# Kernel optimization log

Hardware: AMD Instinct MI355X
Metric: run time of the kernel (lower is better)

Reference implementation:

```python
import jax, jax.numpy as jnp
import numpy as np

INPUTDIM = 256
OUTDIM = 256
GRIDSIZE = 300
SCALE_BASE = 1.0
SCALE_FOURIER = 1.0
BATCH = 2048


def setup_inputs() -> dict:
    key = jax.random.key(0)
    k_x, k_bw, k_fc = jax.random.split(key, 3)
    x = jax.random.normal(k_x, (BATCH, INPUTDIM), dtype=jnp.float32)
    # HeUniform for base_weight: limit = sqrt(6 / fan_in)
    limit = np.sqrt(6.0 / INPUTDIM)
    base_weight = jax.random.uniform(
        k_bw, (INPUTDIM, OUTDIM), dtype=jnp.float32, minval=-limit, maxval=limit)
    stddev = 1.0 / (np.sqrt(INPUTDIM) * np.sqrt(GRIDSIZE))
    fouriercoeffs = (jax.random.normal(k_fc, (2, OUTDIM, INPUTDIM, GRIDSIZE), dtype=jnp.float32)
                     * jnp.float32(stddev))
    return {"x": x, "base_weight": base_weight, "fouriercoeffs": fouriercoeffs}


def reference(x, base_weight, fouriercoeffs):
    # Base path: silu(x @ W)
    base_output = jax.nn.silu(x @ base_weight)  # [B, J]
    # Fourier feature expansion: k = 1..gridsize
    k = jnp.arange(1, GRIDSIZE + 1, dtype=x.dtype)  # [K]
    theta = x[:, :, None] * k[None, None, :]        # [B, I, K]
    c = jnp.cos(theta)
    s = jnp.sin(theta)
    # einsum 'dbik,djik->bj' split into cos and sin parts
    fourier_output = (jnp.einsum('bik,jik->bj', c, fouriercoeffs[0])
                      + jnp.einsum('bik,jik->bj', s, fouriercoeffs[1]))
    return SCALE_BASE * base_output + SCALE_FOURIER * fourier_output
```

## Files before the change

### kernel.cpp

```cpp
#include <hip/hip_runtime.h>
#include <hip/hip_bf16.h>
#include <cstdint>

#define BATCH   2048
#define INDIM   256
#define OUTDIM  256
#define KGRID   300
#define NCHUNK  10

typedef __attribute__((ext_vector_type(4))) float f32x4;
typedef __attribute__((ext_vector_type(8))) short bf16x8;

__device__ __forceinline__ uint32_t pack_bf16x2(float lo, float hi) {
    union { __hip_bfloat162 h; uint32_t u; } cv;
    cv.h = __float22bfloat162_rn(make_float2(lo, hi));
    return cv.u;
}

__device__ __forceinline__ void load_lds16(const void* g, void* l) {
    __builtin_amdgcn_global_load_lds(
        (const __attribute__((address_space(1))) void*)g,
        (__attribute__((address_space(3))) void*)l, 16, 0, 0);
}

#define PACKED_U4 ((size_t)INDIM * NCHUNK * OUTDIM * 8)
#define PACKED_BYTES (PACKED_U4 * 16)

__global__ __launch_bounds__(256) void pack_kernel(
    const float* __restrict__ fc, uint4* __restrict__ pk)
{
    size_t tidg = (size_t)blockIdx.x * 256 + threadIdx.x;
    int sub = tidg & 7;
    int j   = (tidg >> 3) & 255;
    int ich = (int)(tidg >> 11);
    int ch  = ich % NCHUNK;
    int i   = ich / NCHUNK;
    int kb  = ch * 32 + (sub ^ (j & 7)) * 4;
    if (kb > KGRID - 4) kb = KGRID - 4;
    const float* pc = fc + ((size_t)j * INDIM + i) * KGRID + kb;
    const float* ps = pc + (size_t)OUTDIM * INDIM * KGRID;
    float4 vc = *reinterpret_cast<const float4*>(pc);
    float4 vs = *reinterpret_cast<const float4*>(ps);
    uint4 wv;
    wv.x = pack_bf16x2(vc.x, vs.x);
    wv.y = pack_bf16x2(vc.y, vs.y);
    wv.z = pack_bf16x2(vc.z, vs.z);
    wv.w = pack_bf16x2(vc.w, vs.w);
    pk[tidg] = wv;
}

__global__ __launch_bounds__(256, 2) void fourier_dma_kernel(
    const float* __restrict__ x, const uint4* __restrict__ pk,
    float* __restrict__ part)
{
    __shared__ uint4 Abuf[2][128][8];
    __shared__ uint4 Bbuf[2][128][8];

    const int tid = threadIdx.x;
    const int flat = blockIdx.x + (blockIdx.y << 3) + (blockIdx.z << 4);
    const int L  = (flat & 7) * 64 + (flat >> 3);
    const int b0 = (L & 7) * 256;
    const int j0 = ((L >> 3) & 1) * 128;
    const int z  = L >> 4;
    const int i0 = z * 8;

    const int lane = tid & 63, wave = tid >> 6;
    const int wm = wave >> 1, wn = wave & 1;
    const int lrow = lane & 15, lgrp = lane >> 4;
    const int grow = tid >> 1,  gh = tid & 1;
    const int q4 = wave * 4;

    f32x4 acc[2][4][4] = {};
    float thc[2], thn[2], c1[2], s1[2], t2[2];

    thn[0] = x[(size_t)(b0 + grow) * INDIM + i0];
    thn[1] = x[(size_t)(b0 + 128 + grow) * INDIM + i0];

    {
        const uint4* src = pk + ((size_t)(i0 * NCHUNK) * 256 + j0) * 8;
        #pragma unroll
        for (int q = 0; q < 4; ++q)
            load_lds16(src + (q4 + q) * 64 + lane,
                       (char*)&Bbuf[0][0][0] + (q4 + q) * 1024);
    }

    int il = 0, ch = 0;
    #pragma unroll 1
    for (int t = 0; t < 8 * NCHUNK; ++t) {
        if (ch == 0) {
            thc[0] = thn[0]; thc[1] = thn[1];
            #pragma unroll
            for (int m = 0; m < 2; ++m) {
                __sincosf(thc[m], &s1[m], &c1[m]);
                t2[m] = 2.f * c1[m];
            }
            int iln = (il + 1 < 8) ? il + 1 : il;
            thn[0] = x[(size_t)(b0 + grow) * INDIM + i0 + iln];
            thn[1] = x[(size_t)(b0 + 128 + grow) * INDIM + i0 + iln];
        }
        {
            int il2 = il, ch2 = ch + 1;
            if (ch2 == NCHUNK) { ch2 = 0; il2 = (il + 1 < 8) ? il + 1 : il; }
            const uint4* src =
                pk + ((size_t)((i0 + il2) * NCHUNK + ch2) * 256 + j0) * 8;
            char* dst = (char*)&Bbuf[(t + 1) & 1][0][0];
            #pragma unroll
            for (int q = 0; q < 4; ++q)
                load_lds16(src + (q4 + q) * 64 + lane, dst + (q4 + q) * 1024);
        }
        #pragma unroll
        for (int m = 0; m < 2; ++m) {
            const int k0 = ch * 32 + gh * 16;
            float ck, sk;
            __sincosf(thc[m] * (float)(k0 + 1), &sk, &ck);
            float cp = __builtin_fmaf(ck, c1[m],  sk * s1[m]);
            float sp = __builtin_fmaf(sk, c1[m], -ck * s1[m]);
            const int swz = grow & 7;
            #pragma unroll
            for (int c = 0; c < 4; ++c) {
                uint32_t uu[4];
                #pragma unroll
                for (int qq = 0; qq < 4; ++qq) {
                    uu[qq] = pack_bf16x2(ck, sk);
                    float cn = __builtin_fmaf(t2[m], ck, -cp);
                    float sn = __builtin_fmaf(t2[m], sk, -sp);
                    cp = ck; sp = sk; ck = cn; sk = sn;
                }
                if (ch == NCHUNK - 1) {
                    #pragma unroll
                    for (int qq = 0; qq < 4; ++qq)
                        if (k0 + c * 4 + qq >= KGRID) uu[qq] = 0u;
                }
                Abuf[m][grow][(gh * 4 + c) ^ swz] =
                    make_uint4(uu[0], uu[1], uu[2], uu[3]);
            }
        }
        __syncthreads();
        __builtin_amdgcn_s_setprio(1);
        #pragma unroll
        for (int s = 0; s < 2; ++s) {
            bf16x8 bfr[4];
            #pragma unroll
            for (int nf = 0; nf < 4; ++nf) {
                const int jl = wn * 64 + nf * 16 + lrow;
                uint4 tv = Bbuf[t & 1][jl][(s * 4 + lgrp) ^ (jl & 7)];
                bfr[nf] = *reinterpret_cast<bf16x8*>(&tv);
            }
            #pragma unroll
            for (int m = 0; m < 2; ++m) {
                #pragma unroll
                for (int mf = 0; mf < 4; ++mf) {
                    const int rowA = wm * 64 + mf * 16 + lrow;
                    uint4 tv = Abuf[m][rowA][(s * 4 + lgrp) ^ (rowA & 7)];
                    bf16x8 af = *reinterpret_cast<bf16x8*>(&tv);
                    #pragma unroll
                    for (int nf = 0; nf < 4; ++nf)
                        acc[m][mf][nf] = __builtin_amdgcn_mfma_f32_16x16x32_bf16(
                            af, bfr[nf], acc[m][mf][nf], 0, 0, 0);
                }
            }
        }
        __builtin_amdgcn_s_setprio(0);
        __syncthreads();
        if (++ch == NCHUNK) { ch = 0; ++il; }
    }

    float* pws = part + (size_t)z * BATCH * OUTDIM;
    #pragma unroll
    for (int m = 0; m < 2; ++m)
        #pragma unroll
        for (int mf = 0; mf < 4; ++mf)
            #pragma unroll
            for (int nf = 0; nf < 4; ++nf)
                #pragma unroll
                for (int r = 0; r < 4; ++r) {
                    int b = b0 + m * 128 + wm * 64 + mf * 16 + lgrp * 4 + r;
                    int j = j0 + wn * 64 + nf * 16 + lrow;
                    pws[(size_t)b * OUTDIM + j] = acc[m][mf][nf][r];
                }
}

__global__ __launch_bounds__(256, 2) void fourier_kernel_fb(
    const float* __restrict__ x, const float* __restrict__ fc,
    float* __restrict__ ws, int ips)
{
    __shared__ uint4 Abuf[2][128][8];
    __shared__ uint4 Bbuf[128][8];

    const int tid  = threadIdx.x;
    const int b0   = blockIdx.x * 256;
    const int j0   = blockIdx.y * 128;
    const int i0   = blockIdx.z * ips;

    const int lane = tid & 63, wave = tid >> 6;
    const int wm   = wave >> 1, wn = wave & 1;
    const int lrow = lane & 15, lgrp = lane >> 4;
    const int grow = tid >> 1,  gh = tid & 1;

    f32x4 acc[2][4][4] = {};

    #pragma unroll 1
    for (int il = 0; il < ips; ++il) {
        const int i = i0 + il;
        float th[2], c1[2], s1[2], t2[2];
        th[0] = x[(size_t)(b0 + grow)       * INDIM + i];
        th[1] = x[(size_t)(b0 + 128 + grow) * INDIM + i];
        #pragma unroll
        for (int m = 0; m < 2; ++m) {
            __sincosf(th[m], &s1[m], &c1[m]);
            t2[m] = 2.f * c1[m];
        }
        #pragma unroll 1
        for (int ch = 0; ch < NCHUNK; ++ch) {
            #pragma unroll
            for (int r = 0; r < 4; ++r) {
                int flat = r * 256 + tid;
                int jl = flat >> 3, sub = flat & 7;
                int kb = ch * 32 + sub * 4;
                if (kb > KGRID - 4) kb = KGRID - 4;
                const float* pc = fc + ((size_t)(j0 + jl) * INDIM + i) * KGRID + kb;
                const float* ps = pc + (size_t)OUTDIM * INDIM * KGRID;
                float4 vc = *reinterpret_cast<const float4*>(pc);
                float4 vs = *reinterpret_cast<const float4*>(ps);
                uint4 wv;
                wv.x = pack_bf16x2(vc.x, vs.x);
                wv.y = pack_bf16x2(vc.y, vs.y);
                wv.z = pack_bf16x2(vc.z, vs.z);
                wv.w = pack_bf16x2(vc.w, vs.w);
                Bbuf[jl][sub ^ (jl & 7)] = wv;
            }
            #pragma unroll
            for (int m = 0; m < 2; ++m) {
                const int k0 = ch * 32 + gh * 16;
                float ck, sk;
                __sincosf(th[m] * (float)(k0 + 1), &sk, &ck);
                float cp = __builtin_fmaf(ck, c1[m],  sk * s1[m]);
                float sp = __builtin_fmaf(sk, c1[m], -ck * s1[m]);
                const int swz = grow & 7;
                #pragma unroll
                for (int c = 0; c < 4; ++c) {
                    uint32_t uu[4];
                    #pragma unroll
                    for (int qq = 0; qq < 4; ++qq) {
                        const int kidx = k0 + c * 4 + qq;
                        float cc = (kidx < KGRID) ? ck : 0.f;
                        float ss = (kidx < KGRID) ? sk : 0.f;
                        uu[qq] = pack_bf16x2(cc, ss);
                        float cn = __builtin_fmaf(t2[m], ck, -cp);
                        float sn = __builtin_fmaf(t2[m], sk, -sp);
                        cp = ck; sp = sk; ck = cn; sk = sn;
                    }
                    Abuf[m][grow][(gh * 4 + c) ^ swz] =
                        make_uint4(uu[0], uu[1], uu[2], uu[3]);
                }
            }
            __syncthreads();
            #pragma unroll
            for (int s = 0; s < 2; ++s) {
                bf16x8 bfr[4];
                #pragma unroll
                for (int nf = 0; nf < 4; ++nf) {
                    const int jl = wn * 64 + nf * 16 + lrow;
                    uint4 tv = Bbuf[jl][(s * 4 + lgrp) ^ (jl & 7)];
                    bfr[nf] = *reinterpret_cast<bf16x8*>(&tv);
                }
                #pragma unroll
                for (int m = 0; m < 2; ++m) {
                    #pragma unroll
                    for (int mf = 0; mf < 4; ++mf) {
                        const int rowA = wm * 64 + mf * 16 + lrow;
                        uint4 tv = Abuf[m][rowA][(s * 4 + lgrp) ^ (rowA & 7)];
                        bf16x8 af = *reinterpret_cast<bf16x8*>(&tv);
                        #pragma unroll
                        for (int nf = 0; nf < 4; ++nf)
                            acc[m][mf][nf] = __builtin_amdgcn_mfma_f32_16x16x32_bf16(
                                af, bfr[nf], acc[m][mf][nf], 0, 0, 0);
                    }
                }
            }
            __syncthreads();
        }
    }

    float* pws = ws + (size_t)blockIdx.z * BATCH * OUTDIM;
    #pragma unroll
    for (int m = 0; m < 2; ++m)
        #pragma unroll
        for (int mf = 0; mf < 4; ++mf)
            #pragma unroll
            for (int nf = 0; nf < 4; ++nf)
                #pragma unroll
                for (int r = 0; r < 4; ++r) {
                    int b = b0 + m * 128 + wm * 64 + mf * 16 + lgrp * 4 + r;
                    int j = j0 + wn * 64 + nf * 16 + lrow;
                    pws[(size_t)b * OUTDIM + j] = acc[m][mf][nf][r];
                }
}

__global__ __launch_bounds__(256) void combine_kernel(
    const float* __restrict__ x, const float* __restrict__ w,
    const float* __restrict__ part, float* __restrict__ out, int nsplit)
{
    __shared__ float Xs[64][16];
    __shared__ float Wt[16][68];

    const int tid = threadIdx.x;
    const int b0 = blockIdx.x * 64;
    const int j0 = blockIdx.y * 64;
    const int tx = tid & 15, ty = tid >> 4;

    float acc[4][4] = {};

    for (int kb = 0; kb < INDIM; kb += 16) {
        {
            int m = tid >> 2, kq = (tid & 3) * 4;
            float4 v = *reinterpret_cast<const float4*>(
                &x[(size_t)(b0 + m) * INDIM + kb + kq]);
            Xs[m][kq+0] = v.x; Xs[m][kq+1] = v.y; Xs[m][kq+2] = v.z; Xs[m][kq+3] = v.w;
        }
        {
            int kr = tid >> 4, jc = (tid & 15) * 4;
            float4 v = *reinterpret_cast<const float4*>(
                &w[(size_t)(kb + kr) * OUTDIM + j0 + jc]);
            Wt[kr][jc+0] = v.x; Wt[kr][jc+1] = v.y; Wt[kr][jc+2] = v.z; Wt[kr][jc+3] = v.w;
        }
        __syncthreads();
        #pragma unroll
        for (int kk = 0; kk < 16; ++kk) {
            float a[4], b[4];
            #pragma unroll
            for (int q = 0; q < 4; ++q) { a[q] = Xs[ty*4+q][kk]; b[q] = Wt[kk][tx*4+q]; }
            #pragma unroll
            for (int q = 0; q < 4; ++q)
                #pragma unroll
                for (int p = 0; p < 4; ++p)
                    acc[q][p] = __builtin_fmaf(a[q], b[p], acc[q][p]);
        }
        __syncthreads();
    }

    float psum[4][4] = {};
    for (int s = 0; s < nsplit; ++s) {
        const float* base = part + (size_t)s * BATCH * OUTDIM;
        #pragma unroll
        for (int q = 0; q < 4; ++q) {
            float4 pv = *reinterpret_cast<const float4*>(
                &base[(size_t)(b0 + ty*4 + q) * OUTDIM + j0 + tx*4]);
            psum[q][0] += pv.x; psum[q][1] += pv.y;
            psum[q][2] += pv.z; psum[q][3] += pv.w;
        }
    }

    #pragma unroll
    for (int q = 0; q < 4; ++q)
        #pragma unroll
        for (int p = 0; p < 4; ++p) {
            float v = acc[q][p];
            float sv = v / (1.f + __expf(-v));
            out[(size_t)(b0 + ty*4 + q) * OUTDIM + (j0 + tx*4 + p)] =
                sv + psum[q][p];
        }
}

extern "C" void kernel_launch(void* const* d_in, const int* in_sizes, int n_in,
                              void* d_out, int out_size, void* d_ws, size_t ws_size,
                              hipStream_t stream) {
    const float* x  = (const float*)d_in[0];
    const float* bw = (const float*)d_in[1];
    const float* fc = (const float*)d_in[2];
    float* out = (float*)d_out;

    const size_t per = (size_t)BATCH * OUTDIM * sizeof(float);

    if (ws_size >= PACKED_BYTES + 32 * per) {
        uint4* pk   = (uint4*)d_ws;
        float* part = (float*)((char*)d_ws + PACKED_BYTES);
        pack_kernel<<<(int)(PACKED_U4 / 256), 256, 0, stream>>>(fc, pk);
        fourier_dma_kernel<<<dim3(8, 2, 32), 256, 0, stream>>>(x, pk, part);
        combine_kernel<<<dim3(BATCH / 64, OUTDIM / 64), 256, 0, stream>>>(
            x, bw, part, out, 32);
    } else {
        float* part = (float*)d_ws;
        int S = 32;
        while (S > 1 && (size_t)S * per > ws_size) S >>= 1;
        const int ips = INDIM / S;
        fourier_kernel_fb<<<dim3(BATCH / 256, OUTDIM / 128, S), 256, 0, stream>>>(
            x, fc, part, ips);
        combine_kernel<<<dim3(BATCH / 64, OUTDIM / 64), 256, 0, stream>>>(
            x, bw, part, out, S);
    }
}
```

Before: 244.5 us.

## Retile Fourier GEMM to 128 batch rows by full 256 outputs, pack FMA recurrence

Changes the block tile from 256 batch rows by 128 outputs to 128 batch rows by all 256 outputs. Each block now generates cos/sin features for only 128 rows, so the transcendental and recurrence work is no longer repeated across two output-column blocks. The cost is twice the B-operand traffic per block, now streamed for all 256 columns into a larger double-buffered LDS. It also advances the Chebyshev recurrence for cos and sin together with one packed v_pk_fma_f32 per step.

```diff
diff --git a/kernel.cpp b/kernel.cpp
--- a/kernel.cpp
+++ b/kernel.cpp
@@ -9,12 +9,20 @@
 #define NCHUNK  10
 
 typedef __attribute__((ext_vector_type(4))) float f32x4;
+typedef __attribute__((ext_vector_type(2))) float f32x2;
 typedef __attribute__((ext_vector_type(8))) short bf16x8;
 
 __device__ __forceinline__ uint32_t pack_bf16x2(float lo, float hi) {
     union { __hip_bfloat162 h; uint32_t u; } cv;
     cv.h = __float22bfloat162_rn(make_float2(lo, hi));
     return cv.u;
+}
+
+__device__ __forceinline__ f32x2 pk_fma_sub(f32x2 a, f32x2 b, f32x2 c) {
+    f32x2 d;
+    asm("v_pk_fma_f32 %0, %1, %2, %3 neg_lo:[0,0,1] neg_hi:[0,0,1]"
+        : "=v"(d) : "v"(a), "v"(b), "v"(c));
+    return d;
 }
 
 __device__ __forceinline__ void load_lds16(const void* g, void* l) {
@@ -53,14 +61,13 @@
     const float* __restrict__ x, const uint4* __restrict__ pk,
     float* __restrict__ part)
 {
-    __shared__ uint4 Abuf[2][128][8];
-    __shared__ uint4 Bbuf[2][128][8];
+    __shared__ uint4 Abuf[128][8];
+    __shared__ uint4 Bbuf[2][256][8];
 
     const int tid = threadIdx.x;
-    const int flat = blockIdx.x + (blockIdx.y << 3) + (blockIdx.z << 4);
+    const int flat = blockIdx.x + (blockIdx.z << 4);
     const int L  = (flat & 7) * 64 + (flat >> 3);
-    const int b0 = (L & 7) * 256;
-    const int j0 = ((L >> 3) & 1) * 128;
+    const int b0 = (L & 15) * 128;
     const int z  = L >> 4;
     const int i0 = z * 8;
 
@@ -68,70 +75,65 @@
     const int wm = wave >> 1, wn = wave & 1;
     const int lrow = lane & 15, lgrp = lane >> 4;
     const int grow = tid >> 1,  gh = tid & 1;
-    const int q4 = wave * 4;
+    const int q8 = wave * 8;
 
     f32x4 acc[2][4][4] = {};
-    float thc[2], thn[2], c1[2], s1[2], t2[2];
-
-    thn[0] = x[(size_t)(b0 + grow) * INDIM + i0];
-    thn[1] = x[(size_t)(b0 + 128 + grow) * INDIM + i0];
+    float thc, thn, c1v, s1v, t2v;
+
+    thn = x[(size_t)(b0 + grow) * INDIM + i0];
 
     {
-        const uint4* src = pk + ((size_t)(i0 * NCHUNK) * 256 + j0) * 8;
-        #pragma unroll
-        for (int q = 0; q < 4; ++q)
-            load_lds16(src + (q4 + q) * 64 + lane,
-                       (char*)&Bbuf[0][0][0] + (q4 + q) * 1024);
+        const uint4* src = pk + (size_t)(i0 * NCHUNK) * 2048;
+        char* dst = (char*)&Bbuf[0][0][0];
+        #pragma unroll
+        for (int q = 0; q < 8; ++q)
+            load_lds16(src + (q8 + q) * 64 + lane, dst + (q8 + q) * 1024);
     }
 
     int il = 0, ch = 0;
     #pragma unroll 1
     for (int t = 0; t < 8 * NCHUNK; ++t) {
         if (ch == 0) {
-            thc[0] = thn[0]; thc[1] = thn[1];
-            #pragma unroll
-            for (int m = 0; m < 2; ++m) {
-                __sincosf(thc[m], &s1[m], &c1[m]);
-                t2[m] = 2.f * c1[m];
-            }
+            thc = thn;
+            __sincosf(thc, &s1v, &c1v);
+            t2v = 2.f * c1v;
             int iln = (il + 1 < 8) ? il + 1 : il;
-            thn[0] = x[(size_t)(b0 + grow) * INDIM + i0 + iln];
-            thn[1] = x[(size_t)(b0 + 128 + grow) * INDIM + i0 + iln];
+            thn = x[(size_t)(b0 + grow) * INDIM + i0 + iln];
         }
         {
             int il2 = il, ch2 = ch + 1;
             if (ch2 == NCHUNK) { ch2 = 0; il2 = (il + 1 < 8) ? il + 1 : il; }
-            const uint4* src =
-                pk + ((size_t)((i0 + il2) * NCHUNK + ch2) * 256 + j0) * 8;
+            const uint4* src = pk + (size_t)((i0 + il2) * NCHUNK + ch2) * 2048;
             char* dst = (char*)&Bbuf[(t + 1) & 1][0][0];
             #pragma unroll
-            for (int q = 0; q < 4; ++q)
-                load_lds16(src + (q4 + q) * 64 + lane, dst + (q4 + q) * 1024);
-        }
-        #pragma unroll
-        for (int m = 0; m < 2; ++m) {
+            for (int q = 0; q < 8; ++q)
+                load_lds16(src + (q8 + q) * 64 + lane, dst + (q8 + q) * 1024);
+        }
+        {
             const int k0 = ch * 32 + gh * 16;
             float ck, sk;
-            __sincosf(thc[m] * (float)(k0 + 1), &sk, &ck);
-            float cp = __builtin_fmaf(ck, c1[m],  sk * s1[m]);
-            float sp = __builtin_fmaf(sk, c1[m], -ck * s1[m]);
+            __sincosf(thc * (float)(k0 + 1), &sk, &ck);
+            float cp = __builtin_fmaf(ck, c1v,  sk * s1v);
+            float sp = __builtin_fmaf(sk, c1v, -ck * s1v);
+            f32x2 C; C.x = ck; C.y = sk;
+            f32x2 P; P.x = cp; P.y = sp;
+            f32x2 T2; T2.x = t2v; T2.y = t2v;
             const int swz = grow & 7;
             #pragma unroll
             for (int c = 0; c < 4; ++c) {
                 uint32_t uu[4];
                 #pragma unroll
                 for (int qq = 0; qq < 4; ++qq) {
-                    uu[qq] = pack_bf16x2(ck, sk);
-                    float cn = __builtin_fmaf(t2[m], ck, -cp);
-                    float sn = __builtin_fmaf(t2[m], sk, -sp);
-                    cp = ck; sp = sk; ck = cn; sk = sn;
+                    uu[qq] = pack_bf16x2(C.x, C.y);
+                    f32x2 N = pk_fma_sub(T2, C, P);
+                    P = C; C = N;
                 }
                 if (ch == NCHUNK - 1) {
                     #pragma unroll
                     for (int qq = 0; qq < 4; ++qq)
                         if (k0 + c * 4 + qq >= KGRID) uu[qq] = 0u;
                 }
-                Abuf[m][grow][(gh * 4 + c) ^ swz] =
+                Abuf[grow][(gh * 4 + c) ^ swz] =
                     make_uint4(uu[0], uu[1], uu[2], uu[3]);
             }
         }
@@ -139,26 +141,25 @@
         __builtin_amdgcn_s_setprio(1);
         #pragma unroll
         for (int s = 0; s < 2; ++s) {
-            bf16x8 bfr[4];
-            #pragma unroll
-            for (int nf = 0; nf < 4; ++nf) {
-                const int jl = wn * 64 + nf * 16 + lrow;
-                uint4 tv = Bbuf[t & 1][jl][(s * 4 + lgrp) ^ (jl & 7)];
-                bfr[nf] = *reinterpret_cast<bf16x8*>(&tv);
-            }
-            #pragma unroll
-            for (int m = 0; m < 2; ++m) {
-                #pragma unroll
-                for (int mf = 0; mf < 4; ++mf) {
-                    const int rowA = wm * 64 + mf * 16 + lrow;
-                    uint4 tv = Abuf[m][rowA][(s * 4 + lgrp) ^ (rowA & 7)];
-                    bf16x8 af = *reinterpret_cast<bf16x8*>(&tv);
+            bf16x8 afr[4];
+            #pragma unroll
+            for (int mf = 0; mf < 4; ++mf) {
+                const int rowA = wm * 64 + mf * 16 + lrow;
+                uint4 tv = Abuf[rowA][(s * 4 + lgrp) ^ (rowA & 7)];
+                afr[mf] = *reinterpret_cast<bf16x8*>(&tv);
+            }
+            #pragma unroll
+            for (int ns = 0; ns < 2; ++ns)
+                #pragma unroll
+                for (int nf = 0; nf < 4; ++nf) {
+                    const int jl = wn * 128 + ns * 64 + nf * 16 + lrow;
+                    uint4 tv = Bbuf[t & 1][jl][(s * 4 + lgrp) ^ (jl & 7)];
+                    bf16x8 bfr = *reinterpret_cast<bf16x8*>(&tv);
                     #pragma unroll
-                    for (int nf = 0; nf < 4; ++nf)
-                        acc[m][mf][nf] = __builtin_amdgcn_mfma_f32_16x16x32_bf16(
-                            af, bfr[nf], acc[m][mf][nf], 0, 0, 0);
-                }
-            }
+                    for (int mf = 0; mf < 4; ++mf)
+                        acc[ns][mf][nf] = __builtin_amdgcn_mfma_f32_16x16x32_bf16(
+                            afr[mf], bfr, acc[ns][mf][nf], 0, 0, 0);
+                }
         }
         __builtin_amdgcn_s_setprio(0);
         __syncthreads();
@@ -167,16 +168,16 @@
 
     float* pws = part + (size_t)z * BATCH * OUTDIM;
     #pragma unroll
-    for (int m = 0; m < 2; ++m)
+    for (int ns = 0; ns < 2; ++ns)
         #pragma unroll
         for (int mf = 0; mf < 4; ++mf)
             #pragma unroll
             for (int nf = 0; nf < 4; ++nf)
                 #pragma unroll
                 for (int r = 0; r < 4; ++r) {
-                    int b = b0 + m * 128 + wm * 64 + mf * 16 + lgrp * 4 + r;
-                    int j = j0 + wn * 64 + nf * 16 + lrow;
-                    pws[(size_t)b * OUTDIM + j] = acc[m][mf][nf][r];
+                    int b = b0 + wm * 64 + mf * 16 + lgrp * 4 + r;
+                    int j = wn * 128 + ns * 64 + nf * 16 + lrow;
+                    pws[(size_t)b * OUTDIM + j] = acc[ns][mf][nf][r];
                 }
 }
 
@@ -376,7 +377,7 @@
         uint4* pk   = (uint4*)d_ws;
         float* part = (float*)((char*)d_ws + PACKED_BYTES);
         pack_kernel<<<(int)(PACKED_U4 / 256), 256, 0, stream>>>(fc, pk);
-        fourier_dma_kernel<<<dim3(8, 2, 32), 256, 0, stream>>>(x, pk, part);
+        fourier_dma_kernel<<<dim3(16, 1, 32), 256, 0, stream>>>(x, pk, part);
         combine_kernel<<<dim3(BATCH / 64, OUTDIM / 64), 256, 0, stream>>>(
             x, bw, part, out, 32);
     } else {
```

New measurement: 226.3 us. -7.4%, faster.
